# Kernel tuning notes

Hardware: AMD Instinct MI355X
Metric: run time of the kernel (lower is better)

Reference implementation:

```python
import jax, jax.numpy as jnp
import numpy as np

B, S, D, H = 1, 2048, 1280, 16
HD = D // H  # 80


def setup_inputs() -> dict:
    key = jax.random.key(0)
    ks = jax.random.split(key, 6)
    return {
        "hidden_states": jax.random.normal(ks[0], (B, S, D), dtype=jnp.float32),
        "rotary_pos_emb": jax.random.normal(ks[1], (S, HD // 2), dtype=jnp.float32),
        "qkv_w": jax.random.normal(ks[2], (3 * D, D), dtype=jnp.float32) * 0.02,
        "qkv_b": jax.random.normal(ks[3], (3 * D,), dtype=jnp.float32) * 0.02,
        "proj_w": jax.random.normal(ks[4], (D, D), dtype=jnp.float32) * 0.02,
        "proj_b": jax.random.normal(ks[5], (D,), dtype=jnp.float32) * 0.02,
    }


def reference(hidden_states, rotary_pos_emb, qkv_w, qkv_b, proj_w, proj_b):
    b, s, d = hidden_states.shape
    h = H
    hd = d // h
    scaling = hd ** -0.5

    # fused QKV projection: [b, s, 3*d]
    qkv = hidden_states @ qkv_w.T + qkv_b
    qkv = qkv.reshape(b, s, 3, h, hd)
    q, k, v = qkv[:, :, 0], qkv[:, :, 1], qkv[:, :, 2]  # each [b, s, h, hd]

    # rotary embedding: cos/sin [s, hd//2] -> [1, s, 1, hd]
    cos = jnp.cos(rotary_pos_emb)
    sin = jnp.sin(rotary_pos_emb)
    cos = jnp.concatenate([cos, cos], axis=-1)[None, :, None, :]
    sin = jnp.concatenate([sin, sin], axis=-1)[None, :, None, :]

    def apply_rope(x):
        x1, x2 = x[..., : hd // 2], x[..., hd // 2:]
        return x * cos + jnp.concatenate([-x2, x1], axis=-1) * sin

    q = apply_rope(q)
    k = apply_rope(k)

    # [b, h, s, hd]
    q = q.transpose(0, 2, 1, 3)
    k = k.transpose(0, 2, 1, 3)
    v = v.transpose(0, 2, 1, 3)

    # naive full attention matrix [b, h, s, s]
    attn = jnp.einsum("bhqd,bhkd->bhqk", q, k) * scaling
    attn = jax.nn.softmax(attn, axis=-1)
    out = jnp.einsum("bhqk,bhkd->bhqd", attn, v)
    out = out.transpose(0, 2, 1, 3).reshape(b, s, d)
    return out @ proj_w.T + proj_b
```

## Files before the change

### kernel.cpp

```cpp
#include <hip/hip_runtime.h>
#include <math.h>

#define SS 2048
#define DD 1280
#define HH 16
#define HDD 80
#define ND3 3840
#define ZZ 4

typedef __attribute__((ext_vector_type(8))) short short8;
typedef __attribute__((ext_vector_type(4))) short s16x4;
typedef __attribute__((ext_vector_type(4))) float f32x4;
typedef __attribute__((ext_vector_type(8))) _Float16 h16x8;
typedef __attribute__((ext_vector_type(4))) _Float16 h16x4;

__device__ inline short f2bf(float f) {
    union { float f; unsigned u; } x; x.f = f;
    unsigned r = x.u + 0x7FFF + ((x.u >> 16) & 1);
    return (short)(r >> 16);
}

__global__ __launch_bounds__(256) void split_f16(
    const float* __restrict__ a, _Float16* __restrict__ ah, int nbA,
    const float* __restrict__ b, _Float16* __restrict__ bh, int nbB,
    const float* __restrict__ c, _Float16* __restrict__ ch)
{
    const float* x; _Float16* h;
    int blk = blockIdx.x;
    if (blk < nbA)            { x = a; h = ah; }
    else if (blk < nbA + nbB) { blk -= nbA; x = b; h = bh; }
    else                      { blk -= nbA + nbB; x = c; h = ch; }
    int i = (blk * 256 + threadIdx.x) * 4;
    float4 v = *(const float4*)(x + i);
    h16x4 hv;
    hv[0] = (_Float16)v.x; hv[1] = (_Float16)v.y;
    hv[2] = (_Float16)v.z; hv[3] = (_Float16)v.w;
    *(h16x4*)(h + i) = hv;
}

#define LDSA(m, kg) ((m) * 32 + (((kg) ^ (((m) >> 1) & 3)) << 3))

template <int BMT, int BNT>
__global__ __launch_bounds__(256) void gemm_f16(
    const _Float16* __restrict__ Ah, const _Float16* __restrict__ Bh,
    const float* __restrict__ bias, float* __restrict__ C,
    int M, int N, int K)
{
    constexpr int IT = BMT / 32;
    constexpr int JT = BNT / 32;
    constexpr int AU = BMT / 64;
    constexpr int BU = BNT / 64;
    __shared__ _Float16 AhS[BMT * 32];
    __shared__ _Float16 BhS[BNT * 32];

    const int tid = threadIdx.x;
    const int w = tid >> 6;
    const int lane = tid & 63;
    const int l15 = lane & 15;
    const int quad = lane >> 4;
    const int wm = w >> 1, wn = w & 1;
    const int bm = blockIdx.y * BMT;
    const int bn = blockIdx.x * BNT;

    f32x4 acc[IT][JT];
    #pragma unroll
    for (int i = 0; i < IT; ++i)
        #pragma unroll
        for (int j = 0; j < JT; ++j)
            acc[i][j] = (f32x4){0.f, 0.f, 0.f, 0.f};

    h16x8 rah[AU], rbh[BU];
    auto loadg = [&](int k0) {
        #pragma unroll
        for (int u = 0; u < AU; ++u) {
            int c = tid + u * 256, m = c >> 2, kg = c & 3;
            rah[u] = *(const h16x8*)(Ah + (size_t)(bm + m) * K + k0 + kg * 8);
        }
        #pragma unroll
        for (int u = 0; u < BU; ++u) {
            int c = tid + u * 256, m = c >> 2, kg = c & 3;
            rbh[u] = *(const h16x8*)(Bh + (size_t)(bn + m) * K + k0 + kg * 8);
        }
    };

    loadg(0);
    for (int k0 = 0; k0 < K; k0 += 32) {
        __syncthreads();
        #pragma unroll
        for (int u = 0; u < AU; ++u) {
            int c = tid + u * 256, m = c >> 2, kg = c & 3;
            *(h16x8*)&AhS[LDSA(m, kg)] = rah[u];
        }
        #pragma unroll
        for (int u = 0; u < BU; ++u) {
            int c = tid + u * 256, m = c >> 2, kg = c & 3;
            *(h16x8*)&BhS[LDSA(m, kg)] = rbh[u];
        }
        __syncthreads();
        if (k0 + 32 < K) loadg(k0 + 32);

        h16x8 af[IT], bf[JT];
        #pragma unroll
        for (int i = 0; i < IT; ++i) {
            int m = wm * (BMT / 2) + i * 16 + l15;
            af[i] = *(h16x8*)&AhS[LDSA(m, quad)];
        }
        #pragma unroll
        for (int j = 0; j < JT; ++j) {
            int n = wn * (BNT / 2) + j * 16 + l15;
            bf[j] = *(h16x8*)&BhS[LDSA(n, quad)];
        }
        #pragma unroll
        for (int i = 0; i < IT; ++i)
            #pragma unroll
            for (int j = 0; j < JT; ++j)
                acc[i][j] = __builtin_amdgcn_mfma_f32_16x16x32_f16(af[i], bf[j], acc[i][j], 0, 0, 0);
    }

    #pragma unroll
    for (int j = 0; j < JT; ++j) {
        int col = bn + wn * (BNT / 2) + j * 16 + l15;
        float bb = bias[col];
        #pragma unroll
        for (int i = 0; i < IT; ++i)
            #pragma unroll
            for (int r = 0; r < 4; ++r) {
                int row = bm + wm * (BMT / 2) + i * 16 + quad * 4 + r;
                C[(size_t)row * N + col] = acc[i][j][r] + bb;
            }
    }
}

__global__ __launch_bounds__(256) void gemm_proj_merge(
    const _Float16* __restrict__ o_part, const float* __restrict__ l_part,
    const _Float16* __restrict__ Bh,
    const float* __restrict__ bias, float* __restrict__ C,
    int M, int N, int K)
{
    constexpr int BMT = 64, BNT = 128;
    constexpr int JT = BNT / 32;
    constexpr int BU = BNT / 64;
    __shared__ _Float16 AhS[BMT * 32];
    __shared__ _Float16 BhS[BNT * 32];
    __shared__ float linvS[HH * 64];

    const int tid = threadIdx.x;
    const int w = tid >> 6;
    const int lane = tid & 63;
    const int l15 = lane & 15;
    const int quad = lane >> 4;
    const int wm = w >> 1, wn = w & 1;
    const int bm = blockIdx.y * BMT;
    const int bn = blockIdx.x * BNT;

    for (int i = tid; i < HH * 64; i += 256) {
        int h = i >> 6, r = i & 63;
        float ls = 0.f;
        #pragma unroll
        for (int zi = 0; zi < ZZ; ++zi)
            ls += l_part[((size_t)zi * HH + h) * SS + bm + r];
        linvS[i] = 1.f / ls;
    }

    f32x4 acc[2][JT];
    #pragma unroll
    for (int i = 0; i < 2; ++i)
        #pragma unroll
        for (int j = 0; j < JT; ++j)
            acc[i][j] = (f32x4){0.f, 0.f, 0.f, 0.f};

    h16x8 ra[ZZ], rbh[BU];
    auto loadg = [&](int k0) {
        {
            int m = tid >> 2, kg = tid & 3;
            size_t off = (size_t)(bm + m) * K + k0 + kg * 8;
            #pragma unroll
            for (int zi = 0; zi < ZZ; ++zi)
                ra[zi] = *(const h16x8*)(o_part + (size_t)zi * SS * DD + off);
        }
        #pragma unroll
        for (int u = 0; u < BU; ++u) {
            int c = tid + u * 256, m = c >> 2, kg = c & 3;
            rbh[u] = *(const h16x8*)(Bh + (size_t)(bn + m) * K + k0 + kg * 8);
        }
    };

    loadg(0);
    for (int k0 = 0; k0 < K; k0 += 32) {
        __syncthreads();
        {
            int m = tid >> 2, kg = tid & 3;
            int koff = k0 + kg * 8;
            int h = koff / HDD;
            float inv = linvS[h * 64 + m];
            h16x8 f;
            #pragma unroll
            for (int e = 0; e < 8; ++e) {
                float s = (float)ra[0][e];
                #pragma unroll
                for (int zi = 1; zi < ZZ; ++zi) s += (float)ra[zi][e];
                f[e] = (_Float16)(s * inv);
            }
            *(h16x8*)&AhS[LDSA(m, kg)] = f;
        }
        #pragma unroll
        for (int u = 0; u < BU; ++u) {
            int c = tid + u * 256, m = c >> 2, kg = c & 3;
            *(h16x8*)&BhS[LDSA(m, kg)] = rbh[u];
        }
        __syncthreads();
        if (k0 + 32 < K) loadg(k0 + 32);

        h16x8 af[2], bf[JT];
        #pragma unroll
        for (int i = 0; i < 2; ++i) {
            int m = wm * 32 + i * 16 + l15;
            af[i] = *(h16x8*)&AhS[LDSA(m, quad)];
        }
        #pragma unroll
        for (int j = 0; j < JT; ++j) {
            int n = wn * 64 + j * 16 + l15;
            bf[j] = *(h16x8*)&BhS[LDSA(n, quad)];
        }
        #pragma unroll
        for (int i = 0; i < 2; ++i)
            #pragma unroll
            for (int j = 0; j < JT; ++j)
                acc[i][j] = __builtin_amdgcn_mfma_f32_16x16x32_f16(af[i], bf[j], acc[i][j], 0, 0, 0);
    }

    #pragma unroll
    for (int j = 0; j < JT; ++j) {
        int col = bn + wn * 64 + j * 16 + l15;
        float bb = bias[col];
        #pragma unroll
        for (int i = 0; i < 2; ++i)
            #pragma unroll
            for (int r = 0; r < 4; ++r) {
                int row = bm + wm * 32 + i * 16 + quad * 4 + r;
                C[(size_t)row * N + col] = acc[i][j][r] + bb;
            }
    }
}

__global__ __launch_bounds__(256) void rope_scatter_bf16(
    const float* __restrict__ qkv, const float* __restrict__ rpe,
    short* __restrict__ q, short* __restrict__ k, short* __restrict__ v)
{
    __shared__ __align__(16) float cs[40], sn[40];
    const int s = blockIdx.x;
    if (threadIdx.x < 40)
        __sincosf(rpe[s * 40 + threadIdx.x], &sn[threadIdx.x], &cs[threadIdx.x]);
    __syncthreads();
    const float scale = 0.11180339887498949f;
    const float* src = qkv + (size_t)s * ND3;
    for (int t = threadIdx.x; t < ND3 / 4; t += 256) {
        int j4 = t * 4;
        int p = j4 / DD;
        int rem = j4 - p * DD;
        int hh = rem / HDD;
        int d = rem - hh * HDD;
        float4 x = *(const float4*)(src + j4);
        float vv[4];
        if (p == 2) {
            vv[0] = x.x; vv[1] = x.y; vv[2] = x.z; vv[3] = x.w;
        } else {
            bool lo = d < 40;
            int dm = lo ? d : d - 40;
            float4 oth = *(const float4*)(src + p * DD + hh * HDD + (lo ? d + 40 : d - 40));
            float4 c4 = *(const float4*)&cs[dm];
            float4 s4 = *(const float4*)&sn[dm];
            float sg = lo ? -1.f : 1.f;
            vv[0] = x.x * c4.x + sg * oth.x * s4.x;
            vv[1] = x.y * c4.y + sg * oth.y * s4.y;
            vv[2] = x.z * c4.z + sg * oth.z * s4.z;
            vv[3] = x.w * c4.w + sg * oth.w * s4.w;
            if (p == 0) { vv[0] *= scale; vv[1] *= scale; vv[2] *= scale; vv[3] *= scale; }
        }
        short* dst = (p == 0) ? q : (p == 1) ? k : v;
        s16x4 o4;
        o4[0] = f2bf(vv[0]); o4[1] = f2bf(vv[1]);
        o4[2] = f2bf(vv[2]); o4[3] = f2bf(vv[3]);
        *(s16x4*)(dst + ((size_t)hh * SS + s) * HDD + d) = o4;
    }
}

__global__ __launch_bounds__(256) void attn_mfma(
    const short* __restrict__ q, const short* __restrict__ k,
    const short* __restrict__ v, _Float16* __restrict__ o_part,
    float* __restrict__ l_part)
{
    __shared__ short Ks[64][104];
    __shared__ short Vts[80 * 64];
    __shared__ short Ps[4][32 * 64];

    const int h = blockIdx.y;
    const int q0 = blockIdx.x << 7;
    const int z = blockIdx.z;
    const int tid = threadIdx.x;
    const int w = tid >> 6;
    const int lane = tid & 63;
    const int l15 = lane & 15;
    const int quad = lane >> 4;

    const short* qbase = q + (size_t)h * SS * HDD;
    const short* kbase = k + (size_t)h * SS * HDD;
    const short* vbase = v + (size_t)h * SS * HDD;

    short8 qf[2][3];
    #pragma unroll
    for (int i = 0; i < 2; ++i) {
        const int row = q0 + w * 32 + i * 16 + l15;
        #pragma unroll
        for (int kk = 0; kk < 3; ++kk) {
            int c0 = kk * 32 + quad * 8;
            qf[i][kk] = (c0 < HDD) ? *(const short8*)(qbase + (size_t)row * HDD + c0)
                                   : (short8)0;
        }
    }

    if (tid < 128) {
        int r = tid >> 1, c = 80 + (tid & 1) * 8;
        *(short8*)&Ks[r][c] = (short8)0;
    }

    float lsum[2][4] = {{0.f}};
    f32x4 o[2][5];
    #pragma unroll
    for (int i = 0; i < 2; ++i)
        #pragma unroll
        for (int n = 0; n < 5; ++n) o[i][n] = (f32x4){0.f, 0.f, 0.f, 0.f};

    const int kt0 = z << 9;
    for (int kt = kt0; kt < kt0 + 512; kt += 64) {
        __syncthreads();
        #pragma unroll
        for (int u = 0; u < 3; ++u) {
            int i = tid + u * 256;
            if (i < 640) {
                int r = i / 10, c = (i - r * 10) * 8;
                *(short8*)&Ks[r][c] = *(const short8*)(kbase + (size_t)(kt + r) * HDD + c);
            }
        }
        #pragma unroll
        for (int u = 0; u < 2; ++u) {
            int task = tid + u * 256;
            if (task < 320) {
                int r4 = (task & 15) << 2;
                int d4 = (task >> 4) << 2;
                s16x4 a0 = *(const s16x4*)(vbase + (size_t)(kt + r4 + 0) * HDD + d4);
                s16x4 a1 = *(const s16x4*)(vbase + (size_t)(kt + r4 + 1) * HDD + d4);
                s16x4 a2 = *(const s16x4*)(vbase + (size_t)(kt + r4 + 2) * HDD + d4);
                s16x4 a3 = *(const s16x4*)(vbase + (size_t)(kt + r4 + 3) * HDD + d4);
                #pragma unroll
                for (int j = 0; j < 4; ++j) {
                    s16x4 w4 = {a0[j], a1[j], a2[j], a3[j]};
                    int d = d4 + j;
                    int sw = (r4 >> 3) ^ (d & 7);
                    *(s16x4*)&Vts[d * 64 + sw * 8 + (r4 & 7)] = w4;
                }
            }
        }
        __syncthreads();

        f32x4 s_[2][4];
        #pragma unroll
        for (int nt = 0; nt < 4; ++nt) {
            short8 bf0 = *(short8*)&Ks[nt * 16 + l15][quad * 8];
            short8 bf1 = *(short8*)&Ks[nt * 16 + l15][32 + quad * 8];
            short8 bf2 = *(short8*)&Ks[nt * 16 + l15][64 + quad * 8];
            #pragma unroll
            for (int i = 0; i < 2; ++i) {
                f32x4 acc = (f32x4){0.f, 0.f, 0.f, 0.f};
                acc = __builtin_amdgcn_mfma_f32_16x16x32_bf16(qf[i][0], bf0, acc, 0, 0, 0);
                acc = __builtin_amdgcn_mfma_f32_16x16x32_bf16(qf[i][1], bf1, acc, 0, 0, 0);
                acc = __builtin_amdgcn_mfma_f32_16x16x32_bf16(qf[i][2], bf2, acc, 0, 0, 0);
                s_[i][nt] = acc;
            }
        }

        #pragma unroll
        for (int i = 0; i < 2; ++i)
            #pragma unroll
            for (int nt = 0; nt < 4; ++nt)
                #pragma unroll
                for (int r = 0; r < 4; ++r) {
                    float p = __expf(s_[i][nt][r] - 8.f);
                    lsum[i][r] += p;
                    int row = i * 16 + quad * 4 + r;
                    int g = (nt * 2 + (l15 >> 3)) ^ (row & 7);
                    Ps[w][row * 64 + g * 8 + (l15 & 7)] = f2bf(p);
                }

        short8 pf[2][2];
        #pragma unroll
        for (int i = 0; i < 2; ++i)
            #pragma unroll
            for (int kk = 0; kk < 2; ++kk) {
                int g = (kk * 4 + quad) ^ (l15 & 7);
                pf[i][kk] = *(short8*)&Ps[w][(i * 16 + l15) * 64 + g * 8];
            }
        #pragma unroll
        for (int n = 0; n < 5; ++n) {
            #pragma unroll
            for (int kk = 0; kk < 2; ++kk) {
                int d = n * 16 + l15;
                int sw = (kk * 4 + quad) ^ (l15 & 7);
                short8 vf = *(short8*)&Vts[d * 64 + sw * 8];
                #pragma unroll
                for (int i = 0; i < 2; ++i)
                    o[i][n] = __builtin_amdgcn_mfma_f32_16x16x32_bf16(pf[i][kk], vf, o[i][n], 0, 0, 0);
            }
        }
    }

    _Float16* ob = o_part + (size_t)z * SS * DD;
    #pragma unroll
    for (int i = 0; i < 2; ++i) {
        #pragma unroll
        for (int r = 0; r < 4; ++r) {
            float rs = lsum[i][r];
            #pragma unroll
            for (int off = 1; off < 16; off <<= 1)
                rs += __shfl_xor(rs, off, 64);
            lsum[i][r] = rs;
        }
        #pragma unroll
        for (int n = 0; n < 5; ++n)
            #pragma unroll
            for (int r = 0; r < 4; ++r) {
                int row = q0 + w * 32 + i * 16 + quad * 4 + r;
                ob[(size_t)row * DD + h * HDD + n * 16 + l15] = (_Float16)o[i][n][r];
            }
        if (l15 == 0)
            #pragma unroll
            for (int r = 0; r < 4; ++r)
                l_part[((size_t)z * HH + h) * SS + q0 + w * 32 + i * 16 + quad * 4 + r] = lsum[i][r];
    }
}

extern "C" void kernel_launch(void* const* d_in, const int* in_sizes, int n_in,
                              void* d_out, int out_size, void* d_ws, size_t ws_size,
                              hipStream_t stream)
{
    const float* hs     = (const float*)d_in[0];
    const float* rpe    = (const float*)d_in[1];
    const float* qkv_w  = (const float*)d_in[2];
    const float* qkv_b  = (const float*)d_in[3];
    const float* proj_w = (const float*)d_in[4];
    const float* proj_b = (const float*)d_in[5];
    float* out = (float*)d_out;

    short* s0 = (short*)d_ws;
    float* qkv_f  = (float*)d_ws;
    _Float16* o_part = (_Float16*)s0;
    float* l_part = (float*)(s0 + 10485760);
    short* s1 = s0 + 15728640;
    _Float16* qkvw_h = (_Float16*)s1;
    short* qb = s1;
    short* kb = s1 + 2621440;
    short* vb = s1 + 5242880;
    short* s2 = s1 + 7864320;
    _Float16* hs_h = (_Float16*)s2;
    short* s3 = s2 + 2621440;
    _Float16* projw_h = (_Float16*)s3;

    const int n_hs = SS * DD;
    const int n_qw = ND3 * DD;
    const int n_pw = DD * DD;

    split_f16<<<n_hs / 1024 + n_qw / 1024 + n_pw / 1024, 256, 0, stream>>>(
        hs, hs_h, n_hs / 1024,
        qkv_w, qkvw_h, n_qw / 1024,
        proj_w, projw_h);
    gemm_f16<128, 128><<<dim3(ND3 / 128, SS / 128), 256, 0, stream>>>(
        hs_h, qkvw_h, qkv_b, qkv_f, SS, ND3, DD);
    rope_scatter_bf16<<<SS, 256, 0, stream>>>(qkv_f, rpe, qb, kb, vb);
    attn_mfma<<<dim3(SS / 128, HH, ZZ), 256, 0, stream>>>(qb, kb, vb, o_part, l_part);
    gemm_proj_merge<<<dim3(DD / 128, SS / 64), 256, 0, stream>>>(
        o_part, l_part, projw_h, proj_b, out, SS, DD, DD);
}
```

Baseline: 226.1 us.

## Use 8-wave attention blocks with 16 query rows per wave and halve KV splits

The attention kernel moves from 4 waves each handling 32 query rows to 8 waves each handling 16 rows, in 512-thread blocks. The KV split factor drops from 4 to 2, so each block walks 1024 keys. The intent is to lower per-wave register pressure, raise occupancy, spread the shared K/V tile load over more threads and shrink the partial-output traffic the merge GEMM must read. In exchange, each K/V tile loaded to LDS feeds fewer MFMAs per wave, and the grid has half as many blocks.

After: 205.0 us. 1.1x faster.

```diff
diff --git a/kernel.cpp b/kernel.cpp
--- a/kernel.cpp
+++ b/kernel.cpp
@@ -6,7 +6,7 @@
 #define HH 16
 #define HDD 80
 #define ND3 3840
-#define ZZ 4
+#define ZZ 2
 
 typedef __attribute__((ext_vector_type(8))) short short8;
 typedef __attribute__((ext_vector_type(4))) short s16x4;
@@ -285,14 +285,14 @@
     }
 }
 
-__global__ __launch_bounds__(256) void attn_mfma(
+__global__ __launch_bounds__(512, 4) void attn_mfma(
     const short* __restrict__ q, const short* __restrict__ k,
     const short* __restrict__ v, _Float16* __restrict__ o_part,
     float* __restrict__ l_part)
 {
     __shared__ short Ks[64][104];
     __shared__ short Vts[80 * 64];
-    __shared__ short Ps[4][32 * 64];
+    __shared__ short Ps[8][16 * 64];
 
     const int h = blockIdx.y;
     const int q0 = blockIdx.x << 7;
@@ -307,15 +307,14 @@
     const short* kbase = k + (size_t)h * SS * HDD;
     const short* vbase = v + (size_t)h * SS * HDD;
 
-    short8 qf[2][3];
-    #pragma unroll
-    for (int i = 0; i < 2; ++i) {
-        const int row = q0 + w * 32 + i * 16 + l15;
+    short8 qf[3];
+    {
+        const int row = q0 + w * 16 + l15;
         #pragma unroll
         for (int kk = 0; kk < 3; ++kk) {
             int c0 = kk * 32 + quad * 8;
-            qf[i][kk] = (c0 < HDD) ? *(const short8*)(qbase + (size_t)row * HDD + c0)
-                                   : (short8)0;
+            qf[kk] = (c0 < HDD) ? *(const short8*)(qbase + (size_t)row * HDD + c0)
+                                : (short8)0;
         }
     }
 
@@ -324,27 +323,24 @@
         *(short8*)&Ks[r][c] = (short8)0;
     }
 
-    float lsum[2][4] = {{0.f}};
-    f32x4 o[2][5];
-    #pragma unroll
-    for (int i = 0; i < 2; ++i)
-        #pragma unroll
-        for (int n = 0; n < 5; ++n) o[i][n] = (f32x4){0.f, 0.f, 0.f, 0.f};
-
-    const int kt0 = z << 9;
-    for (int kt = kt0; kt < kt0 + 512; kt += 64) {
-        __syncthreads();
-        #pragma unroll
-        for (int u = 0; u < 3; ++u) {
-            int i = tid + u * 256;
+    float lsum[4] = {0.f, 0.f, 0.f, 0.f};
+    f32x4 o[5];
+    #pragma unroll
+    for (int n = 0; n < 5; ++n) o[n] = (f32x4){0.f, 0.f, 0.f, 0.f};
+
+    const int kt0 = z << 10;
+    for (int kt = kt0; kt < kt0 + 1024; kt += 64) {
+        __syncthreads();
+        #pragma unroll
+        for (int u = 0; u < 2; ++u) {
+            int i = tid + u * 512;
             if (i < 640) {
                 int r = i / 10, c = (i - r * 10) * 8;
                 *(short8*)&Ks[r][c] = *(const short8*)(kbase + (size_t)(kt + r) * HDD + c);
             }
         }
-        #pragma unroll
-        for (int u = 0; u < 2; ++u) {
-            int task = tid + u * 256;
+        {
+            int task = tid;
             if (task < 320) {
                 int r4 = (task & 15) << 2;
                 int d4 = (task >> 4) << 2;
@@ -363,43 +359,36 @@
         }
         __syncthreads();
 
-        f32x4 s_[2][4];
+        f32x4 s_[4];
         #pragma unroll
         for (int nt = 0; nt < 4; ++nt) {
             short8 bf0 = *(short8*)&Ks[nt * 16 + l15][quad * 8];
             short8 bf1 = *(short8*)&Ks[nt * 16 + l15][32 + quad * 8];
             short8 bf2 = *(short8*)&Ks[nt * 16 + l15][64 + quad * 8];
-            #pragma unroll
-            for (int i = 0; i < 2; ++i) {
-                f32x4 acc = (f32x4){0.f, 0.f, 0.f, 0.f};
-                acc = __builtin_amdgcn_mfma_f32_16x16x32_bf16(qf[i][0], bf0, acc, 0, 0, 0);
-                acc = __builtin_amdgcn_mfma_f32_16x16x32_bf16(qf[i][1], bf1, acc, 0, 0, 0);
-                acc = __builtin_amdgcn_mfma_f32_16x16x32_bf16(qf[i][2], bf2, acc, 0, 0, 0);
-                s_[i][nt] = acc;
-            }
-        }
-
-        #pragma unroll
-        for (int i = 0; i < 2; ++i)
-            #pragma unroll
-            for (int nt = 0; nt < 4; ++nt)
-                #pragma unroll
-                for (int r = 0; r < 4; ++r) {
-                    float p = __expf(s_[i][nt][r] - 8.f);
-                    lsum[i][r] += p;
-                    int row = i * 16 + quad * 4 + r;
-                    int g = (nt * 2 + (l15 >> 3)) ^ (row & 7);
-                    Ps[w][row * 64 + g * 8 + (l15 & 7)] = f2bf(p);
-                }
-
-        short8 pf[2][2];
-        #pragma unroll
-        for (int i = 0; i < 2; ++i)
-            #pragma unroll
-            for (int kk = 0; kk < 2; ++kk) {
-                int g = (kk * 4 + quad) ^ (l15 & 7);
-                pf[i][kk] = *(short8*)&Ps[w][(i * 16 + l15) * 64 + g * 8];
-            }
+            f32x4 acc = (f32x4){0.f, 0.f, 0.f, 0.f};
+            acc = __builtin_amdgcn_mfma_f32_16x16x32_bf16(qf[0], bf0, acc, 0, 0, 0);
+            acc = __builtin_amdgcn_mfma_f32_16x16x32_bf16(qf[1], bf1, acc, 0, 0, 0);
+            acc = __builtin_amdgcn_mfma_f32_16x16x32_bf16(qf[2], bf2, acc, 0, 0, 0);
+            s_[nt] = acc;
+        }
+
+        #pragma unroll
+        for (int nt = 0; nt < 4; ++nt)
+            #pragma unroll
+            for (int r = 0; r < 4; ++r) {
+                float p = __expf(s_[nt][r] - 8.f);
+                lsum[r] += p;
+                int row = quad * 4 + r;
+                int g = (nt * 2 + (l15 >> 3)) ^ (row & 7);
+                Ps[w][row * 64 + g * 8 + (l15 & 7)] = f2bf(p);
+            }
+
+        short8 pf[2];
+        #pragma unroll
+        for (int kk = 0; kk < 2; ++kk) {
+            int g = (kk * 4 + quad) ^ (l15 & 7);
+            pf[kk] = *(short8*)&Ps[w][l15 * 64 + g * 8];
+        }
         #pragma unroll
         for (int n = 0; n < 5; ++n) {
             #pragma unroll
@@ -407,36 +396,31 @@
                 int d = n * 16 + l15;
                 int sw = (kk * 4 + quad) ^ (l15 & 7);
                 short8 vf = *(short8*)&Vts[d * 64 + sw * 8];
-                #pragma unroll
-                for (int i = 0; i < 2; ++i)
-                    o[i][n] = __builtin_amdgcn_mfma_f32_16x16x32_bf16(pf[i][kk], vf, o[i][n], 0, 0, 0);
+                o[n] = __builtin_amdgcn_mfma_f32_16x16x32_bf16(pf[kk], vf, o[n], 0, 0, 0);
             }
         }
     }
 
     _Float16* ob = o_part + (size_t)z * SS * DD;
     #pragma unroll
-    for (int i = 0; i < 2; ++i) {
+    for (int r = 0; r < 4; ++r) {
+        float rs = lsum[r];
+        #pragma unroll
+        for (int off = 1; off < 16; off <<= 1)
+            rs += __shfl_xor(rs, off, 64);
+        lsum[r] = rs;
+    }
+    #pragma unroll
+    for (int n = 0; n < 5; ++n)
         #pragma unroll
         for (int r = 0; r < 4; ++r) {
-            float rs = lsum[i][r];
-            #pragma unroll
-            for (int off = 1; off < 16; off <<= 1)
-                rs += __shfl_xor(rs, off, 64);
-            lsum[i][r] = rs;
-        }
-        #pragma unroll
-        for (int n = 0; n < 5; ++n)
-            #pragma unroll
-            for (int r = 0; r < 4; ++r) {
-                int row = q0 + w * 32 + i * 16 + quad * 4 + r;
-                ob[(size_t)row * DD + h * HDD + n * 16 + l15] = (_Float16)o[i][n][r];
-            }
-        if (l15 == 0)
-            #pragma unroll
-            for (int r = 0; r < 4; ++r)
-                l_part[((size_t)z * HH + h) * SS + q0 + w * 32 + i * 16 + quad * 4 + r] = lsum[i][r];
-    }
+            int row = q0 + w * 16 + quad * 4 + r;
+            ob[(size_t)row * DD + h * HDD + n * 16 + l15] = (_Float16)o[n][r];
+        }
+    if (l15 == 0)
+        #pragma unroll
+        for (int r = 0; r < 4; ++r)
+            l_part[((size_t)z * HH + h) * SS + q0 + w * 16 + quad * 4 + r] = lsum[r];
 }
 
 extern "C" void kernel_launch(void* const* d_in, const int* in_sizes, int n_in,
@@ -476,7 +460,7 @@
     gemm_f16<128, 128><<<dim3(ND3 / 128, SS / 128), 256, 0, stream>>>(
         hs_h, qkvw_h, qkv_b, qkv_f, SS, ND3, DD);
     rope_scatter_bf16<<<SS, 256, 0, stream>>>(qkv_f, rpe, qb, kb, vb);
-    attn_mfma<<<dim3(SS / 128, HH, ZZ), 256, 0, stream>>>(qb, kb, vb, o_part, l_part);
+    attn_mfma<<<dim3(SS / 128, HH, ZZ), 512, 0, stream>>>(qb, kb, vb, o_part, l_part);
     gemm_proj_merge<<<dim3(DD / 128, SS / 64), 256, 0, stream>>>(
         o_part, l_part, projw_h, proj_b, out, SS, DD, DD);
 }
```
